# Kernel optimization log

Measured on AMD Instinct MI355X. Metric: run time of the kernel, lower is better.

The kernel has to match this reference:

```python
import jax, jax.numpy as jnp
import numpy as np

N0, N1, N2 = 500000, 100000, 20000
E1, E2 = 1600000, 320000
DIN, DH, DOUT = 128, 256, 128
EPS_BN = 1e-5
EPS_NORM = 1e-12


def setup_inputs() -> dict:
    key = jax.random.key(0)
    k = jax.random.split(key, 16)
    s = 0.05
    return {
        "x": jax.random.normal(k[0], (N0, DIN), jnp.float32),
        "src1": jax.random.randint(k[1], (E1,), 0, N0),
        "dst1": jax.random.randint(k[2], (E1,), 0, N1),
        "src2": jax.random.randint(k[3], (E2,), 0, N1),
        "dst2": jax.random.randint(k[4], (E2,), 0, N2),
        "n1": N1,
        "n2": N2,
        "W1_1": jax.random.normal(k[5], (DH, DIN), jnp.float32) * s,
        "W2_1": jax.random.normal(k[6], (DH, DIN), jnp.float32) * s,
        "b2_1": jax.random.normal(k[7], (DH,), jnp.float32) * s,
        "gamma1": jax.random.uniform(k[8], (DH,), jnp.float32, 0.5, 1.5),
        "beta1": jax.random.normal(k[9], (DH,), jnp.float32) * s,
        "mean1": jax.random.normal(k[10], (DH,), jnp.float32) * s,
        "var1": jax.random.uniform(k[11], (DH,), jnp.float32, 0.5, 1.5),
        "W1_2": jax.random.normal(k[12], (DOUT, DH), jnp.float32) * s,
        "W2_2": jax.random.normal(k[13], (DOUT, DH), jnp.float32) * s,
        "b2_2": jax.random.normal(k[14], (DOUT,), jnp.float32) * s,
    }


def _mean_agg(h, src, dst, n_target):
    # torch_sparse.matmul(adj_t, h, reduce='mean'): per-target mean of neighbor rows
    ssum = jax.ops.segment_sum(h[src], dst, num_segments=n_target)
    cnt = jax.ops.segment_sum(jnp.ones(src.shape, h.dtype), dst, num_segments=n_target)
    return ssum / jnp.maximum(cnt, 1.0)[:, None]


def _l2norm(h):
    # F.normalize(h, p=2, dim=1)
    n = jnp.sqrt(jnp.sum(h * h, axis=1, keepdims=True))
    return h / jnp.maximum(n, EPS_NORM)


def reference(x, src1, dst1, src2, dst2, n1, n2,
              W1_1, W2_1, b2_1, gamma1, beta1, mean1, var1,
              W1_2, W2_2, b2_2):
    # --- layer 1: SageConv(in=128, out=256) ---
    h_n = _mean_agg(x, src1, dst1, n1)                 # [n1, DIN]
    h = x[:n1] @ W1_1.T + (h_n @ W2_1.T + b2_1)        # [n1, DH]
    h = _l2norm(h)
    # BatchNorm1d (eval mode: running stats), then ReLU; dropout is identity in eval
    h = gamma1 * (h - mean1) * jax.lax.rsqrt(var1 + EPS_BN) + beta1
    h = jax.nn.relu(h)
    # --- layer 2: SageConv(in=256, out=128) ---
    h_n2 = _mean_agg(h, src2, dst2, n2)                # [n2, DH]
    out = h[:n2] @ W1_2.T + (h_n2 @ W2_2.T + b2_2)     # [n2, DOUT]
    return _l2norm(out)
```

## Files before the change

kernel.cpp:

```cpp
#include <hip/hip_runtime.h>
#include <hip/hip_bf16.h>

#define N1C  100000
#define N2C  20000
#define DIN_ 128
#define DH_  256
#define DOUT_ 128
#define CAP_LOG2 6
#define CAP_     64

typedef unsigned short ushort_t;
typedef unsigned int   uint_t;
typedef __attribute__((ext_vector_type(8))) short bf16x8;
typedef __attribute__((ext_vector_type(4))) float f32x4;

__device__ __forceinline__ float bf2f(ushort_t u) {
    return __uint_as_float(((uint_t)u) << 16);
}
__device__ __forceinline__ ushort_t f2bf(float f) {
    uint_t x = __float_as_uint(f);
    x += 0x7fffu + ((x >> 16) & 1u);
    return (ushort_t)(x >> 16);
}

__global__ __launch_bounds__(256) void convert_all_kernel(
    const float* __restrict__ src, ushort_t* __restrict__ dst, long long n8,
    const float* __restrict__ w0, const float* __restrict__ w1,
    const float* __restrict__ w2, const float* __restrict__ w3,
    ushort_t* __restrict__ wdst)
{
    const long long t = (long long)blockIdx.x * 256 + threadIdx.x;
    if (t < n8) {
        const float4 v0 = *(const float4*)(src + t * 8);
        const float4 v1 = *(const float4*)(src + t * 8 + 4);
        uint4 o;
        o.x = (uint_t)f2bf(v0.x) | ((uint_t)f2bf(v0.y) << 16);
        o.y = (uint_t)f2bf(v0.z) | ((uint_t)f2bf(v0.w) << 16);
        o.z = (uint_t)f2bf(v1.x) | ((uint_t)f2bf(v1.y) << 16);
        o.w = (uint_t)f2bf(v1.z) | ((uint_t)f2bf(v1.w) << 16);
        *(uint4*)(dst + t * 8) = o;
    } else {
        const long long t2 = t - n8;
        if (t2 >= 16384) return;
        const int mat = (int)(t2 >> 12);
        const long long idx = (long long)(t2 & 4095) * 8;
        const float* s = (mat == 0) ? w0 : (mat == 1) ? w1 : (mat == 2) ? w2 : w3;
        const float4 v0 = *(const float4*)(s + idx);
        const float4 v1 = *(const float4*)(s + idx + 4);
        uint4 o;
        o.x = (uint_t)f2bf(v0.x) | ((uint_t)f2bf(v0.y) << 16);
        o.y = (uint_t)f2bf(v0.z) | ((uint_t)f2bf(v0.w) << 16);
        o.z = (uint_t)f2bf(v1.x) | ((uint_t)f2bf(v1.y) << 16);
        o.w = (uint_t)f2bf(v1.z) | ((uint_t)f2bf(v1.w) << 16);
        *(uint4*)(wdst + (long long)mat * 32768 + idx) = o;
    }
}

__global__ __launch_bounds__(256) void scatter_bucket_kernel(
    const int* __restrict__ src1, const int* __restrict__ dst1, int E1,
    const int* __restrict__ src2, const int* __restrict__ dst2, int E2,
    int* __restrict__ cnt1, int* __restrict__ esrc1,
    int* __restrict__ cnt2, int* __restrict__ esrc2)
{
    const int t = blockIdx.x * 256 + threadIdx.x;
    if (t < E1) {
        const int s = src1[t];
        const int d = dst1[t];
        const int p = atomicAdd(&cnt1[d], 1);
        if (p < CAP_) esrc1[((size_t)d << CAP_LOG2) + p] = s;
    } else if (t < E1 + E2) {
        const int e = t - E1;
        const int s = src2[e];
        const int d = dst2[e];
        const int p = atomicAdd(&cnt2[d], 1);
        if (p < CAP_) esrc2[((size_t)d << CAP_LOG2) + p] = s;
    }
}

__global__ __launch_bounds__(256) void gather_mean_128_bf16(
    const ushort_t* __restrict__ X, const int* __restrict__ cnt,
    const int* __restrict__ esrc, ushort_t* __restrict__ agg, int n)
{
    const int w = (blockIdx.x * 256 + threadIdx.x) >> 6;
    const int lane = threadIdx.x & 63;
    if (w >= n) return;
    const int deg = cnt[w];
    const int end = (deg < CAP_) ? deg : CAP_;
    const int* ep = esrc + ((size_t)w << CAP_LOG2);
    const int c = lane << 1;
    float ax = 0.f, ay = 0.f;
    int e = 0;
    for (; e + 3 < end; e += 4) {
        const int s0 = ep[e], s1 = ep[e+1], s2 = ep[e+2], s3 = ep[e+3];
        const uint_t u0 = *(const uint_t*)(X + (size_t)s0 * DIN_ + c);
        const uint_t u1 = *(const uint_t*)(X + (size_t)s1 * DIN_ + c);
        const uint_t u2 = *(const uint_t*)(X + (size_t)s2 * DIN_ + c);
        const uint_t u3 = *(const uint_t*)(X + (size_t)s3 * DIN_ + c);
        ax += bf2f((ushort_t)u0) + bf2f((ushort_t)u1)
            + bf2f((ushort_t)u2) + bf2f((ushort_t)u3);
        ay += bf2f((ushort_t)(u0 >> 16)) + bf2f((ushort_t)(u1 >> 16))
            + bf2f((ushort_t)(u2 >> 16)) + bf2f((ushort_t)(u3 >> 16));
    }
    for (; e < end; ++e) {
        const uint_t u0 = *(const uint_t*)(X + (size_t)ep[e] * DIN_ + c);
        ax += bf2f((ushort_t)u0);
        ay += bf2f((ushort_t)(u0 >> 16));
    }
    const float r = 1.0f / fmaxf((float)deg, 1.0f);
    const uint_t o = (uint_t)f2bf(ax * r) | ((uint_t)f2bf(ay * r) << 16);
    *(uint_t*)(agg + (size_t)w * DIN_ + c) = o;
}

__global__ __launch_bounds__(256) void gather_mean_256_bf16(
    const ushort_t* __restrict__ X, const int* __restrict__ cnt,
    const int* __restrict__ esrc, ushort_t* __restrict__ agg, int n)
{
    const int w = (blockIdx.x * 256 + threadIdx.x) >> 6;
    const int lane = threadIdx.x & 63;
    if (w >= n) return;
    const int deg = cnt[w];
    const int end = (deg < CAP_) ? deg : CAP_;
    const int* ep = esrc + ((size_t)w << CAP_LOG2);
    const int c = lane << 2;
    float a0 = 0.f, a1 = 0.f, a2 = 0.f, a3 = 0.f;
    int e = 0;
    for (; e + 3 < end; e += 4) {
        const int s0 = ep[e], s1 = ep[e+1], s2 = ep[e+2], s3 = ep[e+3];
        const uint2 u0 = *(const uint2*)(X + (size_t)s0 * DH_ + c);
        const uint2 u1 = *(const uint2*)(X + (size_t)s1 * DH_ + c);
        const uint2 u2 = *(const uint2*)(X + (size_t)s2 * DH_ + c);
        const uint2 u3 = *(const uint2*)(X + (size_t)s3 * DH_ + c);
        a0 += bf2f((ushort_t)u0.x) + bf2f((ushort_t)u1.x)
            + bf2f((ushort_t)u2.x) + bf2f((ushort_t)u3.x);
        a1 += bf2f((ushort_t)(u0.x >> 16)) + bf2f((ushort_t)(u1.x >> 16))
            + bf2f((ushort_t)(u2.x >> 16)) + bf2f((ushort_t)(u3.x >> 16));
        a2 += bf2f((ushort_t)u0.y) + bf2f((ushort_t)u1.y)
            + bf2f((ushort_t)u2.y) + bf2f((ushort_t)u3.y);
        a3 += bf2f((ushort_t)(u0.y >> 16)) + bf2f((ushort_t)(u1.y >> 16))
            + bf2f((ushort_t)(u2.y >> 16)) + bf2f((ushort_t)(u3.y >> 16));
    }
    for (; e < end; ++e) {
        const uint2 u0 = *(const uint2*)(X + (size_t)ep[e] * DH_ + c);
        a0 += bf2f((ushort_t)u0.x);
        a1 += bf2f((ushort_t)(u0.x >> 16));
        a2 += bf2f((ushort_t)u0.y);
        a3 += bf2f((ushort_t)(u0.y >> 16));
    }
    const float r = 1.0f / fmaxf((float)deg, 1.0f);
    uint2 o;
    o.x = (uint_t)f2bf(a0 * r) | ((uint_t)f2bf(a1 * r) << 16);
    o.y = (uint_t)f2bf(a2 * r) | ((uint_t)f2bf(a3 * r) << 16);
    *(uint2*)(agg + (size_t)w * DH_ + c) = o;
}

__global__ __launch_bounds__(256) void gemm1_fused(
    const ushort_t* __restrict__ A1, const ushort_t* __restrict__ B1,
    const ushort_t* __restrict__ A2, const ushort_t* __restrict__ B2,
    const float* __restrict__ bias,
    const float* __restrict__ gamma, const float* __restrict__ beta,
    const float* __restrict__ mean, const float* __restrict__ var,
    ushort_t* __restrict__ H, int M)
{
    __shared__ ushort_t As[64][40];
    __shared__ ushort_t Bs[256][40];
    __shared__ float rowss[4][64];

    const int tid = threadIdx.x;
    const int m0 = blockIdx.x * 64;

    const int ar = tid >> 2;
    const int aq = (tid & 3) * 8;
    const bool arow_ok = (m0 + ar) < M;

    const int wid  = tid >> 6;
    const int lane = tid & 63;
    const int lm   = lane & 15;
    const int lqq  = lane >> 4;
    const int wcol = wid * 64;

    const f32x4 fzero = {0.f, 0.f, 0.f, 0.f};
    f32x4 acc[4][4];
    #pragma unroll
    for (int i = 0; i < 4; ++i)
        #pragma unroll
        for (int j = 0; j < 4; ++j) acc[i][j] = fzero;

    #pragma unroll
    for (int phase = 0; phase < 2; ++phase) {
        const ushort_t* __restrict__ A = phase ? A2 : A1;
        const ushort_t* __restrict__ B = phase ? B2 : B1;
        const ushort_t* Ap = A + (size_t)(m0 + ar) * 128 + aq;
        const ushort_t* Bp = B + (size_t)tid * 128;

        #pragma unroll
        for (int k0 = 0; k0 < 128; k0 += 32) {
            uint4 a = {0, 0, 0, 0};
            if (arow_ok) a = *(const uint4*)(Ap + k0);
            const uint4 b0 = *(const uint4*)(Bp + k0);
            const uint4 b1 = *(const uint4*)(Bp + k0 + 8);
            const uint4 b2 = *(const uint4*)(Bp + k0 + 16);
            const uint4 b3 = *(const uint4*)(Bp + k0 + 24);

            __syncthreads();
            *(uint4*)&As[ar][aq]   = a;
            *(uint4*)&Bs[tid][0]   = b0;
            *(uint4*)&Bs[tid][8]   = b1;
            *(uint4*)&Bs[tid][16]  = b2;
            *(uint4*)&Bs[tid][24]  = b3;
            __syncthreads();

            bf16x8 af[4], bfr[4];
            #pragma unroll
            for (int i = 0; i < 4; ++i)
                af[i] = *(const bf16x8*)&As[i * 16 + lm][lqq * 8];
            #pragma unroll
            for (int j = 0; j < 4; ++j)
                bfr[j] = *(const bf16x8*)&Bs[wcol + j * 16 + lm][lqq * 8];

            #pragma unroll
            for (int i = 0; i < 4; ++i)
                #pragma unroll
                for (int j = 0; j < 4; ++j)
                    acc[i][j] = __builtin_amdgcn_mfma_f32_16x16x32_bf16(
                        af[i], bfr[j], acc[i][j], 0, 0, 0);
        }
    }

    float bj[4], sc[4], sh[4];
    #pragma unroll
    for (int j = 0; j < 4; ++j) {
        const int C = wcol + j * 16 + lm;
        bj[j] = bias[C];
        const float is = rsqrtf(var[C] + 1e-5f);
        sc[j] = gamma[C] * is;
        sh[j] = beta[C] - mean[C] * gamma[C] * is;
    }

    float ss[4][4];
    #pragma unroll
    for (int i = 0; i < 4; ++i) {
        #pragma unroll
        for (int r = 0; r < 4; ++r) {
            float s = 0.f;
            #pragma unroll
            for (int j = 0; j < 4; ++j) {
                const float v = acc[i][j][r] + bj[j];
                acc[i][j][r] = v;
                s += v * v;
            }
            s += __shfl_xor(s, 1);
            s += __shfl_xor(s, 2);
            s += __shfl_xor(s, 4);
            s += __shfl_xor(s, 8);
            ss[i][r] = s;
        }
    }
    if (lm == 0) {
        #pragma unroll
        for (int i = 0; i < 4; ++i)
            #pragma unroll
            for (int r = 0; r < 4; ++r)
                rowss[wid][i * 16 + lqq * 4 + r] = ss[i][r];
    }
    __syncthreads();

    #pragma unroll
    for (int i = 0; i < 4; ++i) {
        #pragma unroll
        for (int r = 0; r < 4; ++r) {
            const int R = i * 16 + lqq * 4 + r;
            const float tot = rowss[0][R] + rowss[1][R] + rowss[2][R] + rowss[3][R];
            const float inv = 1.0f / fmaxf(sqrtf(tot), 1e-12f);
            const int row = m0 + R;
            if (row < M) {
                const size_t base = (size_t)row * DH_ + wcol + lm;
                #pragma unroll
                for (int j = 0; j < 4; ++j) {
                    const float v = fmaxf(acc[i][j][r] * inv * sc[j] + sh[j], 0.f);
                    H[base + j * 16] = f2bf(v);
                }
            }
        }
    }
}

__global__ __launch_bounds__(256) void gemm2_fused(
    const ushort_t* __restrict__ A1, const ushort_t* __restrict__ B1,
    const ushort_t* __restrict__ A2, const ushort_t* __restrict__ B2,
    const float* __restrict__ bias,
    float* __restrict__ Cout, int M)
{
    __shared__ ushort_t As[128][40];
    __shared__ ushort_t Bs[128][40];
    __shared__ float rowss[2][128];

    const int tid = threadIdx.x;
    const int m0 = blockIdx.x * 128;

    const int lr = tid >> 1;
    const int lq = (tid & 1) * 8;

    const int wid  = tid >> 6;
    const int lane = tid & 63;
    const int lm   = lane & 15;
    const int lqq  = lane >> 4;
    const int wrow = (wid >> 1) * 64;
    const int wcol = (wid & 1) * 64;
    const int wc   = wid & 1;

    const f32x4 fzero = {0.f, 0.f, 0.f, 0.f};
    f32x4 acc[4][4];
    #pragma unroll
    for (int i = 0; i < 4; ++i)
        #pragma unroll
        for (int j = 0; j < 4; ++j) acc[i][j] = fzero;

    const bool arow_ok = (m0 + lr) < M;

    #pragma unroll
    for (int phase = 0; phase < 2; ++phase) {
        const ushort_t* __restrict__ A = phase ? A2 : A1;
        const ushort_t* __restrict__ B = phase ? B2 : B1;
        const ushort_t* Ap = A + (size_t)(m0 + lr) * 256 + lq;
        const ushort_t* Bp = B + (size_t)lr * 256 + lq;

        for (int k0 = 0; k0 < 256; k0 += 32) {
            uint4 a0 = {0, 0, 0, 0}, a1 = {0, 0, 0, 0};
            if (arow_ok) {
                a0 = *(const uint4*)(Ap + k0);
                a1 = *(const uint4*)(Ap + k0 + 16);
            }
            const uint4 b0 = *(const uint4*)(Bp + k0);
            const uint4 b1 = *(const uint4*)(Bp + k0 + 16);

            __syncthreads();
            *(uint4*)&As[lr][lq]      = a0;
            *(uint4*)&As[lr][lq + 16] = a1;
            *(uint4*)&Bs[lr][lq]      = b0;
            *(uint4*)&Bs[lr][lq + 16] = b1;
            __syncthreads();

            bf16x8 af[4], bfr[4];
            #pragma unroll
            for (int i = 0; i < 4; ++i)
                af[i] = *(const bf16x8*)&As[wrow + i * 16 + lm][lqq * 8];
            #pragma unroll
            for (int j = 0; j < 4; ++j)
                bfr[j] = *(const bf16x8*)&Bs[wcol + j * 16 + lm][lqq * 8];

            #pragma unroll
            for (int i = 0; i < 4; ++i)
                #pragma unroll
                for (int j = 0; j < 4; ++j)
                    acc[i][j] = __builtin_amdgcn_mfma_f32_16x16x32_bf16(
                        af[i], bfr[j], acc[i][j], 0, 0, 0);
        }
    }

    float bj[4];
    #pragma unroll
    for (int j = 0; j < 4; ++j) bj[j] = bias[wcol + j * 16 + lm];

    float ss[4][4];
    #pragma unroll
    for (int i = 0; i < 4; ++i) {
        #pragma unroll
        for (int r = 0; r < 4; ++r) {
            float s = 0.f;
            #pragma unroll
            for (int j = 0; j < 4; ++j) {
                const float v = acc[i][j][r] + bj[j];
                acc[i][j][r] = v;
                s += v * v;
            }
            s += __shfl_xor(s, 1);
            s += __shfl_xor(s, 2);
            s += __shfl_xor(s, 4);
            s += __shfl_xor(s, 8);
            ss[i][r] = s;
        }
    }
    if (lm == 0) {
        #pragma unroll
        for (int i = 0; i < 4; ++i)
            #pragma unroll
            for (int r = 0; r < 4; ++r)
                rowss[wc][wrow + i * 16 + lqq * 4 + r] = ss[i][r];
    }
    __syncthreads();

    #pragma unroll
    for (int i = 0; i < 4; ++i) {
        #pragma unroll
        for (int r = 0; r < 4; ++r) {
            const int R = wrow + i * 16 + lqq * 4 + r;
            const float tot = rowss[0][R] + rowss[1][R];
            const float inv = 1.0f / fmaxf(sqrtf(tot), 1e-12f);
            const int row = m0 + R;
            if (row < M) {
                const size_t base = (size_t)row * DOUT_ + wcol + lm;
                #pragma unroll
                for (int j = 0; j < 4; ++j)
                    Cout[base + j * 16] = acc[i][j][r] * inv;
            }
        }
    }
}

extern "C" void kernel_launch(void* const* d_in, const int* in_sizes, int n_in,
                              void* d_out, int out_size, void* d_ws, size_t ws_size,
                              hipStream_t stream)
{
    const float* x     = (const float*)d_in[0];
    const int*   src1  = (const int*)d_in[1];
    const int*   dst1  = (const int*)d_in[2];
    const int*   src2  = (const int*)d_in[3];
    const int*   dst2  = (const int*)d_in[4];
    const float* W1_1  = (const float*)d_in[7];
    const float* W2_1  = (const float*)d_in[8];
    const float* b2_1  = (const float*)d_in[9];
    const float* gamma1= (const float*)d_in[10];
    const float* beta1 = (const float*)d_in[11];
    const float* mean1 = (const float*)d_in[12];
    const float* var1  = (const float*)d_in[13];
    const float* W1_2  = (const float*)d_in[14];
    const float* W2_2  = (const float*)d_in[15];
    const float* b2_2  = (const float*)d_in[16];
    float* out = (float*)d_out;

    const int E1 = in_sizes[1];
    const int E2 = in_sizes[3];
    const int n1 = N1C;
    const int n2 = N2C;

    char* wsb = (char*)d_ws;
    ushort_t* xb    = (ushort_t*)(wsb + 0);
    ushort_t* h     = (ushort_t*)(wsb + 128000000);
    ushort_t* agg1  = (ushort_t*)(wsb + 179200000);
    ushort_t* agg2  = (ushort_t*)(wsb + 204800000);
    int*      esrc1 = (int*)(wsb + 215040000);
    int*      esrc2 = (int*)(wsb + 240640000);
    int*      cnt1  = (int*)(wsb + 245760000);
    int*      cnt2  = (int*)(wsb + 246160000);
    ushort_t* wb    = (ushort_t*)(wsb + 246240000);
    ushort_t* w11b = wb;
    ushort_t* w21b = wb + 32768;
    ushort_t* w12b = wb + 65536;
    ushort_t* w22b = wb + 98304;

    {
        const long long n8 = (long long)500000 * DIN_ / 8;
        const int nblk = (int)(n8 / 256) + 64;
        convert_all_kernel<<<nblk, 256, 0, stream>>>(x, xb, n8,
                                                     W1_1, W2_1, W1_2, W2_2, wb);
    }

    hipMemsetAsync(cnt1, 0, 480000, stream);
    {
        const int tE = E1 + E2;
        scatter_bucket_kernel<<<(tE + 255) / 256, 256, 0, stream>>>(
            src1, dst1, E1, src2, dst2, E2, cnt1, esrc1, cnt2, esrc2);
    }

    gather_mean_128_bf16<<<(n1 + 3) / 4, 256, 0, stream>>>(xb, cnt1, esrc1, agg1, n1);
    gemm1_fused<<<(n1 + 63) / 64, 256, 0, stream>>>(
        xb, w11b, agg1, w21b, b2_1, gamma1, beta1, mean1, var1, h, n1);

    gather_mean_256_bf16<<<(n2 + 3) / 4, 256, 0, stream>>>(h, cnt2, esrc2, agg2, n2);
    gemm2_fused<<<(n2 + 127) / 128, 256, 0, stream>>>(
        h, w12b, agg2, w22b, b2_2, out, n2);
}
```

Baseline: 719.7 us.

## Replace global-atomic edge scatter with two-pass binned bucket build in LDS

The single scatter kernel, which did one global atomic per edge on a per-destination counter and wrote scattered entries, is replaced by two passes. The first pass bins edges by destination blocks of 128 using a shared-memory histogram, a scan and one global atomic per bin per chunk, and writes bin-contiguous staged pairs. The second pass builds each bin's 128x64 bucket table in LDS and writes it out with coalesced int4 stores, along with the counts. This removes the contention and scatter of global atomics, but adds an extra kernel, an extra round trip through global memory, and a fixed per-bin capacity (3072 edges) that could silently drop edges on skewed inputs.

```diff
diff --git a/kernel.cpp b/kernel.cpp
--- a/kernel.cpp
+++ b/kernel.cpp
@@ -8,6 +8,13 @@
 #define DOUT_ 128
 #define CAP_LOG2 6
 #define CAP_     64
+
+#define BIN_SHIFT 7
+#define NBIN1 782
+#define NBIN2 157
+#define NBINS 939
+#define CAP_BIN 3072
+#define CHUNK_A 8192
 
 typedef unsigned short ushort_t;
 typedef unsigned int   uint_t;
@@ -56,25 +63,123 @@
     }
 }
 
-__global__ __launch_bounds__(256) void scatter_bucket_kernel(
+__global__ __launch_bounds__(256) void bin_edges_kernel(
     const int* __restrict__ src1, const int* __restrict__ dst1, int E1,
     const int* __restrict__ src2, const int* __restrict__ dst2, int E2,
+    int* __restrict__ gTail, uint2* __restrict__ binBuf)
+{
+    __shared__ int hist[NBINS];
+    __shared__ int binOff[NBINS];
+    __shared__ int runc[NBINS];
+    __shared__ int gb[NBINS];
+    __shared__ uint2 stage[CHUNK_A];
+    __shared__ int wtot[4];
+
+    const int tid = threadIdx.x;
+    const int tE = E1 + E2;
+    const int c0 = blockIdx.x * CHUNK_A;
+    const int cend = (c0 + CHUNK_A < tE) ? (c0 + CHUNK_A) : tE;
+    const int ccnt = cend - c0;
+
+    for (int b = tid; b < NBINS; b += 256) hist[b] = 0;
+    __syncthreads();
+
+    for (int i = c0 + tid; i < cend; i += 256) {
+        int d, bin;
+        if (i < E1) { d = dst1[i];      bin = d >> BIN_SHIFT; }
+        else        { d = dst2[i - E1]; bin = NBIN1 + (d >> BIN_SHIFT); }
+        atomicAdd(&hist[bin], 1);
+    }
+    __syncthreads();
+
+    {
+        int h[4]; int tsum = 0;
+        #pragma unroll
+        for (int k = 0; k < 4; ++k) {
+            const int b = tid * 4 + k;
+            h[k] = (b < NBINS) ? hist[b] : 0;
+            tsum += h[k];
+        }
+        int s = tsum;
+        #pragma unroll
+        for (int o = 1; o < 64; o <<= 1) {
+            int t = __shfl_up(s, (unsigned)o);
+            if ((tid & 63) >= o) s += t;
+        }
+        if ((tid & 63) == 63) wtot[tid >> 6] = s;
+        __syncthreads();
+        int wpre = 0;
+        #pragma unroll
+        for (int k = 0; k < 4; ++k) wpre += (k < (tid >> 6)) ? wtot[k] : 0;
+        int run = wpre + (s - tsum);
+        #pragma unroll
+        for (int k = 0; k < 4; ++k) {
+            const int b = tid * 4 + k;
+            if (b < NBINS) {
+                binOff[b] = run;
+                runc[b]   = run;
+                gb[b] = h[k] ? atomicAdd(&gTail[b], h[k]) : 0;
+            }
+            run += h[k];
+        }
+    }
+    __syncthreads();
+
+    for (int i = c0 + tid; i < cend; i += 256) {
+        int s, d, bin;
+        if (i < E1) { s = src1[i];      d = dst1[i];      bin = d >> BIN_SHIFT; }
+        else        { s = src2[i - E1]; d = dst2[i - E1]; bin = NBIN1 + (d >> BIN_SHIFT); }
+        const int r = atomicAdd(&runc[bin], 1);
+        stage[r] = make_uint2((uint_t)s, (uint_t)d | ((uint_t)bin << 17));
+    }
+    __syncthreads();
+
+    for (int i = tid; i < ccnt; i += 256) {
+        const uint2 u = stage[i];
+        const int bin = (int)(u.y >> 17);
+        const int local = gb[bin] + (i - binOff[bin]);
+        if (local < CAP_BIN)
+            binBuf[(size_t)bin * CAP_BIN + local] = u;
+    }
+}
+
+__global__ __launch_bounds__(256) void build_buckets_kernel(
+    const int* __restrict__ gTail, const uint2* __restrict__ binBuf,
     int* __restrict__ cnt1, int* __restrict__ esrc1,
     int* __restrict__ cnt2, int* __restrict__ esrc2)
 {
-    const int t = blockIdx.x * 256 + threadIdx.x;
-    if (t < E1) {
-        const int s = src1[t];
-        const int d = dst1[t];
-        const int p = atomicAdd(&cnt1[d], 1);
-        if (p < CAP_) esrc1[((size_t)d << CAP_LOG2) + p] = s;
-    } else if (t < E1 + E2) {
-        const int e = t - E1;
-        const int s = src2[e];
-        const int d = dst2[e];
-        const int p = atomicAdd(&cnt2[d], 1);
-        if (p < CAP_) esrc2[((size_t)d << CAP_LOG2) + p] = s;
-    }
+    __shared__ int run[128];
+    __shared__ int eLDS[128 * CAP_];
+
+    const int b = blockIdx.x;
+    const int tid = threadIdx.x;
+    const int t0 = gTail[b];
+    const int nE = (t0 < CAP_BIN) ? t0 : CAP_BIN;
+    const bool g2 = (b >= NBIN1);
+    const int lb = g2 ? (b - NBIN1) : b;
+    const int d0 = lb << BIN_SHIFT;
+    const int n  = g2 ? N2C : N1C;
+    int* cnt  = g2 ? cnt2  : cnt1;
+    int* esrc = g2 ? esrc2 : esrc1;
+
+    for (int k = tid; k < 128; k += 256) run[k] = 0;
+    __syncthreads();
+
+    const uint2* bp = binBuf + (size_t)b * CAP_BIN;
+    for (int i = tid; i < nE; i += 256) {
+        const uint2 u = bp[i];
+        const int ld = (int)(u.y & 127u);
+        const int slot = atomicAdd(&run[ld], 1);
+        if (slot < CAP_) eLDS[(ld << CAP_LOG2) + slot] = (int)u.x;
+    }
+    __syncthreads();
+
+    const int nd = ((n - d0) < 128) ? (n - d0) : 128;
+    const int tot4 = (nd << CAP_LOG2) >> 2;
+    int4* dstp = (int4*)(esrc + ((size_t)d0 << CAP_LOG2));
+    const int4* srcp = (const int4*)eLDS;
+    for (int i = tid; i < tot4; i += 256) dstp[i] = srcp[i];
+    for (int k = tid; k < nd; k += 256) cnt[d0 + k] = run[k];
 }
 
 __global__ __launch_bounds__(256) void gather_mean_128_bf16(
@@ -434,15 +539,17 @@
     const int n2 = N2C;
 
     char* wsb = (char*)d_ws;
-    ushort_t* xb    = (ushort_t*)(wsb + 0);
-    ushort_t* h     = (ushort_t*)(wsb + 128000000);
-    ushort_t* agg1  = (ushort_t*)(wsb + 179200000);
-    ushort_t* agg2  = (ushort_t*)(wsb + 204800000);
-    int*      esrc1 = (int*)(wsb + 215040000);
-    int*      esrc2 = (int*)(wsb + 240640000);
-    int*      cnt1  = (int*)(wsb + 245760000);
-    int*      cnt2  = (int*)(wsb + 246160000);
-    ushort_t* wb    = (ushort_t*)(wsb + 246240000);
+    ushort_t* xb     = (ushort_t*)(wsb + 0);
+    ushort_t* h      = (ushort_t*)(wsb + 128000000);
+    ushort_t* agg1   = (ushort_t*)(wsb + 179200000);
+    ushort_t* agg2   = (ushort_t*)(wsb + 204800000);
+    int*      esrc1  = (int*)(wsb + 215040000);
+    int*      esrc2  = (int*)(wsb + 240640000);
+    int*      cnt1   = (int*)(wsb + 245760000);
+    int*      cnt2   = (int*)(wsb + 246160000);
+    ushort_t* wb     = (ushort_t*)(wsb + 246240000);
+    int*      gTail  = (int*)(wsb + 246502400);
+    uint2*    binBuf = (uint2*)(wsb + 246507520);
     ushort_t* w11b = wb;
     ushort_t* w21b = wb + 32768;
     ushort_t* w12b = wb + 65536;
@@ -455,11 +562,14 @@
                                                      W1_1, W2_1, W1_2, W2_2, wb);
     }
 
-    hipMemsetAsync(cnt1, 0, 480000, stream);
+    hipMemsetAsync(gTail, 0, NBINS * sizeof(int), stream);
     {
         const int tE = E1 + E2;
-        scatter_bucket_kernel<<<(tE + 255) / 256, 256, 0, stream>>>(
-            src1, dst1, E1, src2, dst2, E2, cnt1, esrc1, cnt2, esrc2);
+        const int nblkA = (tE + CHUNK_A - 1) / CHUNK_A;
+        bin_edges_kernel<<<nblkA, 256, 0, stream>>>(
+            src1, dst1, E1, src2, dst2, E2, gTail, binBuf);
+        build_buckets_kernel<<<NBINS, 256, 0, stream>>>(
+            gTail, binBuf, cnt1, esrc1, cnt2, esrc2);
     }
 
     gather_mean_128_bf16<<<(n1 + 3) / 4, 256, 0, stream>>>(xb, cnt1, esrc1, agg1, n1);
```

Measured after the change: 651.1 us. 9.5% less time.
